# Performance work log

Measured on AMD Instinct MI355X. Metric: run time of the kernel, lower is better.

Reference implementation:

```python
import jax, jax.numpy as jnp
import numpy as np

N = 8192
F_IN = 256
F_OUT = 128
ALPHA = 0.2  # leaky relu slope
NEG_INF = -9e15


def setup_inputs() -> dict:
    key = jax.random.key(0)
    k_x, k_w, k_a, k_adj = jax.random.split(key, 4)
    x = jax.random.normal(k_x, (N, F_IN), dtype=jnp.float32)
    # xavier_uniform for W
    limit = np.sqrt(6.0 / (F_IN + F_OUT)).astype(np.float32)
    W = jax.random.uniform(k_w, (F_IN, F_OUT), minval=-limit, maxval=limit, dtype=jnp.float32)
    a = jax.random.normal(k_a, (2 * F_OUT, 1), dtype=jnp.float32) * 0.1
    adj = (jax.random.uniform(k_adj, (N, N)) < 0.01).astype(jnp.float32)
    adj = jnp.maximum(adj, jnp.eye(N, dtype=jnp.float32))
    return {"x": x, "adj": adj, "W": W, "a": a}


def reference(x, adj, W, a):
    # h = X W : [N, F_OUT]
    h = x @ W
    # e_ij = leakyrelu([h_i || h_j] . a) = leakyrelu((h a1)_i + (h a2)_j)
    a1 = a[:F_OUT, 0]  # [F_OUT]
    a2 = a[F_OUT:, 0]  # [F_OUT]
    e = (h @ a1)[:, None] + (h @ a2)[None, :]  # [N, N]
    e = jnp.where(e > 0, e, ALPHA * e)  # LeakyReLU
    att = jnp.where(adj > 0.0, e, NEG_INF)
    att = jax.nn.softmax(att, axis=1)  # row softmax over neighbors
    # dropout p=0.0 -> identity
    h_prime = att @ h  # [N, F_OUT]
    # concat=True -> ELU
    return jax.nn.elu(h_prime)
```

## Files before the change

kernel.cpp:

```cpp
#include <hip/hip_runtime.h>
#include <math.h>

#define N 8192
#define F_IN 256
#define F_OUT 128
#define ALPHA 0.2f
#define CAP 256
#define GEMM_BLOCKS 256

typedef float f32x4 __attribute__((ext_vector_type(4)));

__global__ __launch_bounds__(256) void fused_gemm_scan(const float* __restrict__ x,
                                                       const float* __restrict__ W,
                                                       const float* __restrict__ a,
                                                       const float* __restrict__ adj,
                                                       float* __restrict__ h,
                                                       float* __restrict__ s1,
                                                       float* __restrict__ s2,
                                                       unsigned short* __restrict__ idx,
                                                       int* __restrict__ cnt) {
    __shared__ float xst[64][36];

    const int t = threadIdx.x;
    if (blockIdx.x < GEMM_BLOCKS) {
        const int row0 = blockIdx.x * 32;
        const int rg = t >> 5;
        const int cg = t & 31;
        float acc[4][4] = {};

        for (int k0 = 0; k0 < F_IN; k0 += 64) {
            #pragma unroll
            for (int i = 0; i < 2; ++i) {
                int fi = t + i * 256;
                int r  = fi >> 4;
                int c4 = fi & 15;
                float4 v = *(const float4*)(&x[(size_t)(row0 + r) * F_IN + k0 + c4 * 4]);
                xst[c4 * 4 + 0][r] = v.x;
                xst[c4 * 4 + 1][r] = v.y;
                xst[c4 * 4 + 2][r] = v.z;
                xst[c4 * 4 + 3][r] = v.w;
            }
            __syncthreads();
            #pragma unroll 8
            for (int kk = 0; kk < 64; ++kk) {
                float4 wv = *(const float4*)(&W[(size_t)(k0 + kk) * F_OUT + cg * 4]);
                float4 xv = *(const float4*)(&xst[kk][rg * 4]);
                acc[0][0] += xv.x * wv.x; acc[0][1] += xv.x * wv.y;
                acc[0][2] += xv.x * wv.z; acc[0][3] += xv.x * wv.w;
                acc[1][0] += xv.y * wv.x; acc[1][1] += xv.y * wv.y;
                acc[1][2] += xv.y * wv.z; acc[1][3] += xv.y * wv.w;
                acc[2][0] += xv.z * wv.x; acc[2][1] += xv.z * wv.y;
                acc[2][2] += xv.z * wv.z; acc[2][3] += xv.z * wv.w;
                acc[3][0] += xv.w * wv.x; acc[3][1] += xv.w * wv.y;
                acc[3][2] += xv.w * wv.z; acc[3][3] += xv.w * wv.w;
            }
            __syncthreads();
        }
        #pragma unroll
        for (int r = 0; r < 4; ++r) {
            float4 v = make_float4(acc[r][0], acc[r][1], acc[r][2], acc[r][3]);
            *(float4*)(&h[(size_t)(row0 + rg * 4 + r) * F_OUT + cg * 4]) = v;
        }
        float4 a1 = *(const float4*)(&a[cg * 4]);
        float4 a2 = *(const float4*)(&a[F_OUT + cg * 4]);
        #pragma unroll
        for (int r = 0; r < 4; ++r) {
            float v1 = acc[r][0] * a1.x + acc[r][1] * a1.y + acc[r][2] * a1.z + acc[r][3] * a1.w;
            float v2 = acc[r][0] * a2.x + acc[r][1] * a2.y + acc[r][2] * a2.z + acc[r][3] * a2.w;
            #pragma unroll
            for (int o = 16; o > 0; o >>= 1) {
                v1 += __shfl_xor(v1, o);
                v2 += __shfl_xor(v2, o);
            }
            if (((t & 63) & 31) == 0) {
                s1[row0 + rg * 4 + r] = v1;
                s2[row0 + rg * 4 + r] = v2;
            }
        }
    } else {
        const int wave = t >> 6;
        const int lane = t & 63;
        const int row = (blockIdx.x - GEMM_BLOCKS) * 4 + wave;
        const f32x4* __restrict__ arow = (const f32x4*)(adj + (size_t)row * N);
        unsigned short* __restrict__ outp = idx + (size_t)row * CAP;
        const unsigned long long lt = (1ULL << lane) - 1ULL;
        int c = 0;
        for (int it = 0; it < 32; it += 8) {
            f32x4 vv[8];
            #pragma unroll
            for (int q = 0; q < 8; ++q)
                vv[q] = __builtin_nontemporal_load(&arow[(it + q) * 64 + lane]);
            #pragma unroll
            for (int q = 0; q < 8; ++q) {
                const int base = ((it + q) * 64 + lane) * 4;
                #pragma unroll
                for (int u = 0; u < 4; ++u) {
                    float val = vv[q][u];
                    unsigned long long m = __ballot(val > 0.0f);
                    if (val > 0.0f) {
                        int pos = c + __popcll(m & lt);
                        if (pos < CAP) outp[pos] = (unsigned short)(base + u);
                    }
                    c += (int)__popcll(m);
                }
            }
        }
        if (lane == 0) cnt[row] = c;
    }
}

__global__ __launch_bounds__(256) void attn_gather(const unsigned short* __restrict__ idx,
                                                   const int* __restrict__ cnt,
                                                   const float* __restrict__ h,
                                                   const float* __restrict__ s1,
                                                   const float* __restrict__ s2,
                                                   float* __restrict__ out) {
    __shared__ float wv[CAP];
    __shared__ unsigned short js[CAP];
    __shared__ float red1[4], red2[4];
    __shared__ float pacc[8][128];

    const int i = blockIdx.x;
    const int t = threadIdx.x;
    const int lane = t & 63;
    const int wave = t >> 6;
    const int K = min(cnt[i], CAP);

    float e = -INFINITY;
    int j = 0;
    if (t < K) {
        j = idx[(size_t)i * CAP + t];
        float v = s1[i] + s2[j];
        e = v > 0.0f ? v : ALPHA * v;
    }
    float m = e;
    #pragma unroll
    for (int o = 32; o > 0; o >>= 1) m = fmaxf(m, __shfl_xor(m, o));
    if (lane == 0) red1[wave] = m;
    __syncthreads();
    m = fmaxf(fmaxf(red1[0], red1[1]), fmaxf(red1[2], red1[3]));

    float w = (t < K) ? expf(e - m) : 0.0f;
    float s = w;
    #pragma unroll
    for (int o = 32; o > 0; o >>= 1) s += __shfl_xor(s, o);
    if (lane == 0) red2[wave] = s;
    wv[t] = w;
    js[t] = (unsigned short)j;
    __syncthreads();
    const float invl = 1.0f / (red2[0] + red2[1] + red2[2] + red2[3]);

    const int g   = t >> 5;
    const int l32 = t & 31;
    const float4* __restrict__ h4 = (const float4*)h;
    float ax = 0.0f, ay = 0.0f, az = 0.0f, aw = 0.0f;
    int k = g;
    for (; k + 8 < K; k += 16) {
        float w0 = wv[k];     int j0 = js[k];
        float w1 = wv[k + 8]; int j1 = js[k + 8];
        float4 h0 = h4[(size_t)j0 * 32 + l32];
        float4 h1 = h4[(size_t)j1 * 32 + l32];
        ax += w0 * h0.x + w1 * h1.x;
        ay += w0 * h0.y + w1 * h1.y;
        az += w0 * h0.z + w1 * h1.z;
        aw += w0 * h0.w + w1 * h1.w;
    }
    for (; k < K; k += 8) {
        float w0 = wv[k]; int j0 = js[k];
        float4 h0 = h4[(size_t)j0 * 32 + l32];
        ax += w0 * h0.x; ay += w0 * h0.y; az += w0 * h0.z; aw += w0 * h0.w;
    }
    pacc[g][l32 * 4 + 0] = ax;
    pacc[g][l32 * 4 + 1] = ay;
    pacc[g][l32 * 4 + 2] = az;
    pacc[g][l32 * 4 + 3] = aw;
    __syncthreads();

    if (t < 128) {
        float v = pacc[0][t] + pacc[1][t] + pacc[2][t] + pacc[3][t]
                + pacc[4][t] + pacc[5][t] + pacc[6][t] + pacc[7][t];
        v *= invl;
        v = v > 0.0f ? v : expm1f(v);
        out[(size_t)i * F_OUT + t] = v;
    }
}

extern "C" void kernel_launch(void* const* d_in, const int* in_sizes, int n_in,
                              void* d_out, int out_size, void* d_ws, size_t ws_size,
                              hipStream_t stream) {
    const float* x   = (const float*)d_in[0];
    const float* adj = (const float*)d_in[1];
    const float* W   = (const float*)d_in[2];
    const float* a   = (const float*)d_in[3];
    float* out = (float*)d_out;

    float* h  = (float*)d_ws;
    float* s1 = h + (size_t)N * F_OUT;
    float* s2 = s1 + N;
    int*   cnt = (int*)(s2 + N);
    unsigned short* idx = (unsigned short*)(cnt + N);

    fused_gemm_scan<<<GEMM_BLOCKS + N / 4, 256, 0, stream>>>(x, W, a, adj, h, s1, s2, idx, cnt);
    attn_gather<<<N, 256, 0, stream>>>(idx, cnt, h, s1, s2, out);
}
```

Measured before the change: 379.3 us.

## Fuse adjacency scan with attention gather, one row per wave

Splits the GEMM into its own kernel and fuses the adjacency scan with softmax and aggregation in a single kernel. Each wave handles one row, keeping neighbor indices and weights in shared memory. This removes the global idx/cnt buffers and the separate per-row gather launch. In exchange, the scan no longer overlaps the GEMM, and each row's gather uses fewer threads.

```diff
diff --git a/kernel.cpp b/kernel.cpp
--- a/kernel.cpp
+++ b/kernel.cpp
@@ -6,158 +6,152 @@
 #define F_OUT 128
 #define ALPHA 0.2f
 #define CAP 256
-#define GEMM_BLOCKS 256
 
 typedef float f32x4 __attribute__((ext_vector_type(4)));
 
-__global__ __launch_bounds__(256) void fused_gemm_scan(const float* __restrict__ x,
-                                                       const float* __restrict__ W,
-                                                       const float* __restrict__ a,
-                                                       const float* __restrict__ adj,
-                                                       float* __restrict__ h,
-                                                       float* __restrict__ s1,
-                                                       float* __restrict__ s2,
-                                                       unsigned short* __restrict__ idx,
-                                                       int* __restrict__ cnt) {
+__global__ __launch_bounds__(256) void gemm_xw(const float* __restrict__ x,
+                                               const float* __restrict__ W,
+                                               const float* __restrict__ a,
+                                               float* __restrict__ h,
+                                               float* __restrict__ s1,
+                                               float* __restrict__ s2) {
     __shared__ float xst[64][36];
 
     const int t = threadIdx.x;
-    if (blockIdx.x < GEMM_BLOCKS) {
-        const int row0 = blockIdx.x * 32;
-        const int rg = t >> 5;
-        const int cg = t & 31;
-        float acc[4][4] = {};
+    const int row0 = blockIdx.x * 32;
+    const int rg = t >> 5;
+    const int cg = t & 31;
+    float acc[4][4] = {};
 
-        for (int k0 = 0; k0 < F_IN; k0 += 64) {
-            #pragma unroll
-            for (int i = 0; i < 2; ++i) {
-                int fi = t + i * 256;
-                int r  = fi >> 4;
-                int c4 = fi & 15;
-                float4 v = *(const float4*)(&x[(size_t)(row0 + r) * F_IN + k0 + c4 * 4]);
-                xst[c4 * 4 + 0][r] = v.x;
-                xst[c4 * 4 + 1][r] = v.y;
-                xst[c4 * 4 + 2][r] = v.z;
-                xst[c4 * 4 + 3][r] = v.w;
-            }
-            __syncthreads();
-            #pragma unroll 8
-            for (int kk = 0; kk < 64; ++kk) {
-                float4 wv = *(const float4*)(&W[(size_t)(k0 + kk) * F_OUT + cg * 4]);
-                float4 xv = *(const float4*)(&xst[kk][rg * 4]);
-                acc[0][0] += xv.x * wv.x; acc[0][1] += xv.x * wv.y;
-                acc[0][2] += xv.x * wv.z; acc[0][3] += xv.x * wv.w;
-                acc[1][0] += xv.y * wv.x; acc[1][1] += xv.y * wv.y;
-                acc[1][2] += xv.y * wv.z; acc[1][3] += xv.y * wv.w;
-                acc[2][0] += xv.z * wv.x; acc[2][1] += xv.z * wv.y;
-                acc[2][2] += xv.z * wv.z; acc[2][3] += xv.z * wv.w;
-                acc[3][0] += xv.w * wv.x; acc[3][1] += xv.w * wv.y;
-                acc[3][2] += xv.w * wv.z; acc[3][3] += xv.w * wv.w;
-            }
-            __syncthreads();
+    for (int k0 = 0; k0 < F_IN; k0 += 64) {
+        #pragma unroll
+        for (int i = 0; i < 2; ++i) {
+            int fi = t + i * 256;
+            int r  = fi >> 4;
+            int c4 = fi & 15;
+            float4 v = *(const float4*)(&x[(size_t)(row0 + r) * F_IN + k0 + c4 * 4]);
+            xst[c4 * 4 + 0][r] = v.x;
+            xst[c4 * 4 + 1][r] = v.y;
+            xst[c4 * 4 + 2][r] = v.z;
+            xst[c4 * 4 + 3][r] = v.w;
         }
+        __syncthreads();
+        #pragma unroll 8
+        for (int kk = 0; kk < 64; ++kk) {
+            float4 wv = *(const float4*)(&W[(size_t)(k0 + kk) * F_OUT + cg * 4]);
+            float4 xv = *(const float4*)(&xst[kk][rg * 4]);
+            acc[0][0] += xv.x * wv.x; acc[0][1] += xv.x * wv.y;
+            acc[0][2] += xv.x * wv.z; acc[0][3] += xv.x * wv.w;
+            acc[1][0] += xv.y * wv.x; acc[1][1] += xv.y * wv.y;
+            acc[1][2] += xv.y * wv.z; acc[1][3] += xv.y * wv.w;
+            acc[2][0] += xv.z * wv.x; acc[2][1] += xv.z * wv.y;
+            acc[2][2] += xv.z * wv.z; acc[2][3] += xv.z * wv.w;
+            acc[3][0] += xv.w * wv.x; acc[3][1] += xv.w * wv.y;
+            acc[3][2] += xv.w * wv.z; acc[3][3] += xv.w * wv.w;
+        }
+        __syncthreads();
+    }
+    #pragma unroll
+    for (int r = 0; r < 4; ++r) {
+        float4 v = make_float4(acc[r][0], acc[r][1], acc[r][2], acc[r][3]);
+        *(float4*)(&h[(size_t)(row0 + rg * 4 + r) * F_OUT + cg * 4]) = v;
+    }
+    float4 a1 = *(const float4*)(&a[cg * 4]);
+    float4 a2 = *(const float4*)(&a[F_OUT + cg * 4]);
+    #pragma unroll
+    for (int r = 0; r < 4; ++r) {
+        float v1 = acc[r][0] * a1.x + acc[r][1] * a1.y + acc[r][2] * a1.z + acc[r][3] * a1.w;
+        float v2 = acc[r][0] * a2.x + acc[r][1] * a2.y + acc[r][2] * a2.z + acc[r][3] * a2.w;
         #pragma unroll
-        for (int r = 0; r < 4; ++r) {
-            float4 v = make_float4(acc[r][0], acc[r][1], acc[r][2], acc[r][3]);
-            *(float4*)(&h[(size_t)(row0 + rg * 4 + r) * F_OUT + cg * 4]) = v;
+        for (int o = 16; o > 0; o >>= 1) {
+            v1 += __shfl_xor(v1, o);
+            v2 += __shfl_xor(v2, o);
         }
-        float4 a1 = *(const float4*)(&a[cg * 4]);
-        float4 a2 = *(const float4*)(&a[F_OUT + cg * 4]);
-        #pragma unroll
-        for (int r = 0; r < 4; ++r) {
-            float v1 = acc[r][0] * a1.x + acc[r][1] * a1.y + acc[r][2] * a1.z + acc[r][3] * a1.w;
-            float v2 = acc[r][0] * a2.x + acc[r][1] * a2.y + acc[r][2] * a2.z + acc[r][3] * a2.w;
-            #pragma unroll
-            for (int o = 16; o > 0; o >>= 1) {
-                v1 += __shfl_xor(v1, o);
-                v2 += __shfl_xor(v2, o);
-            }
-            if (((t & 63) & 31) == 0) {
-                s1[row0 + rg * 4 + r] = v1;
-                s2[row0 + rg * 4 + r] = v2;
-            }
+        if ((t & 31) == 0) {
+            s1[row0 + rg * 4 + r] = v1;
+            s2[row0 + rg * 4 + r] = v2;
         }
-    } else {
-        const int wave = t >> 6;
-        const int lane = t & 63;
-        const int row = (blockIdx.x - GEMM_BLOCKS) * 4 + wave;
-        const f32x4* __restrict__ arow = (const f32x4*)(adj + (size_t)row * N);
-        unsigned short* __restrict__ outp = idx + (size_t)row * CAP;
-        const unsigned long long lt = (1ULL << lane) - 1ULL;
-        int c = 0;
-        for (int it = 0; it < 32; it += 8) {
-            f32x4 vv[8];
-            #pragma unroll
-            for (int q = 0; q < 8; ++q)
-                vv[q] = __builtin_nontemporal_load(&arow[(it + q) * 64 + lane]);
-            #pragma unroll
-            for (int q = 0; q < 8; ++q) {
-                const int base = ((it + q) * 64 + lane) * 4;
-                #pragma unroll
-                for (int u = 0; u < 4; ++u) {
-                    float val = vv[q][u];
-                    unsigned long long m = __ballot(val > 0.0f);
-                    if (val > 0.0f) {
-                        int pos = c + __popcll(m & lt);
-                        if (pos < CAP) outp[pos] = (unsigned short)(base + u);
-                    }
-                    c += (int)__popcll(m);
-                }
-            }
-        }
-        if (lane == 0) cnt[row] = c;
     }
 }
 
-__global__ __launch_bounds__(256) void attn_gather(const unsigned short* __restrict__ idx,
-                                                   const int* __restrict__ cnt,
-                                                   const float* __restrict__ h,
-                                                   const float* __restrict__ s1,
-                                                   const float* __restrict__ s2,
-                                                   float* __restrict__ out) {
-    __shared__ float wv[CAP];
-    __shared__ unsigned short js[CAP];
-    __shared__ float red1[4], red2[4];
-    __shared__ float pacc[8][128];
+__global__ __launch_bounds__(256) void scan_attn(const float* __restrict__ adj,
+                                                 const float* __restrict__ h,
+                                                 const float* __restrict__ s1,
+                                                 const float* __restrict__ s2,
+                                                 float* __restrict__ out) {
+    __shared__ unsigned short js[4][CAP];
+    __shared__ float wv[4][CAP];
 
-    const int i = blockIdx.x;
-    const int t = threadIdx.x;
-    const int lane = t & 63;
-    const int wave = t >> 6;
-    const int K = min(cnt[i], CAP);
+    const int wave = threadIdx.x >> 6;
+    const int lane = threadIdx.x & 63;
+    const int row = blockIdx.x * 4 + wave;
+    const f32x4* __restrict__ arow = (const f32x4*)(adj + (size_t)row * N);
+    const unsigned long long lt = (1ULL << lane) - 1ULL;
 
-    float e = -INFINITY;
-    int j = 0;
-    if (t < K) {
-        j = idx[(size_t)i * CAP + t];
-        float v = s1[i] + s2[j];
-        e = v > 0.0f ? v : ALPHA * v;
+    int c = 0;
+    for (int it = 0; it < 32; it += 8) {
+        f32x4 vv[8];
+        #pragma unroll
+        for (int q = 0; q < 8; ++q)
+            vv[q] = __builtin_nontemporal_load(&arow[(it + q) * 64 + lane]);
+        #pragma unroll
+        for (int q = 0; q < 8; ++q) {
+            const int base = ((it + q) * 64 + lane) * 4;
+            #pragma unroll
+            for (int u = 0; u < 4; ++u) {
+                float val = vv[q][u];
+                unsigned long long m = __ballot(val > 0.0f);
+                if (val > 0.0f) {
+                    int pos = c + __popcll(m & lt);
+                    if (pos < CAP) js[wave][pos] = (unsigned short)(base + u);
+                }
+                c += (int)__popcll(m);
+            }
+        }
     }
-    float m = e;
+    const int K = min(c, CAP);
+    __syncthreads();
+
+    const float s1i = s1[row];
+    float e[4];
+    float mloc = -INFINITY;
     #pragma unroll
-    for (int o = 32; o > 0; o >>= 1) m = fmaxf(m, __shfl_xor(m, o));
-    if (lane == 0) red1[wave] = m;
+    for (int u = 0; u < 4; ++u) {
+        int p = lane + 64 * u;
+        e[u] = -INFINITY;
+        if (p < K) {
+            int j = js[wave][p];
+            float v = s1i + s2[j];
+            v = v > 0.0f ? v : ALPHA * v;
+            e[u] = v;
+            mloc = fmaxf(mloc, v);
+        }
+    }
+    #pragma unroll
+    for (int o = 32; o > 0; o >>= 1) mloc = fmaxf(mloc, __shfl_xor(mloc, o));
+    float ssum = 0.0f;
+    #pragma unroll
+    for (int u = 0; u < 4; ++u) {
+        int p = lane + 64 * u;
+        if (p < K) {
+            float w = expf(e[u] - mloc);
+            wv[wave][p] = w;
+            ssum += w;
+        }
+    }
+    #pragma unroll
+    for (int o = 32; o > 0; o >>= 1) ssum += __shfl_xor(ssum, o);
+    const float invl = 1.0f / ssum;
     __syncthreads();
-    m = fmaxf(fmaxf(red1[0], red1[1]), fmaxf(red1[2], red1[3]));
 
-    float w = (t < K) ? expf(e - m) : 0.0f;
-    float s = w;
-    #pragma unroll
-    for (int o = 32; o > 0; o >>= 1) s += __shfl_xor(s, o);
-    if (lane == 0) red2[wave] = s;
-    wv[t] = w;
-    js[t] = (unsigned short)j;
-    __syncthreads();
-    const float invl = 1.0f / (red2[0] + red2[1] + red2[2] + red2[3]);
-
-    const int g   = t >> 5;
-    const int l32 = t & 31;
+    const int g   = lane >> 5;
+    const int l32 = lane & 31;
     const float4* __restrict__ h4 = (const float4*)h;
     float ax = 0.0f, ay = 0.0f, az = 0.0f, aw = 0.0f;
     int k = g;
-    for (; k + 8 < K; k += 16) {
-        float w0 = wv[k];     int j0 = js[k];
-        float w1 = wv[k + 8]; int j1 = js[k + 8];
+    for (; k + 2 < K; k += 4) {
+        float w0 = wv[wave][k];     int j0 = js[wave][k];
+        float w1 = wv[wave][k + 2]; int j1 = js[wave][k + 2];
         float4 h0 = h4[(size_t)j0 * 32 + l32];
         float4 h1 = h4[(size_t)j1 * 32 + l32];
         ax += w0 * h0.x + w1 * h1.x;
@@ -165,23 +159,22 @@
         az += w0 * h0.z + w1 * h1.z;
         aw += w0 * h0.w + w1 * h1.w;
     }
-    for (; k < K; k += 8) {
-        float w0 = wv[k]; int j0 = js[k];
+    for (; k < K; k += 2) {
+        float w0 = wv[wave][k]; int j0 = js[wave][k];
         float4 h0 = h4[(size_t)j0 * 32 + l32];
         ax += w0 * h0.x; ay += w0 * h0.y; az += w0 * h0.z; aw += w0 * h0.w;
     }
-    pacc[g][l32 * 4 + 0] = ax;
-    pacc[g][l32 * 4 + 1] = ay;
-    pacc[g][l32 * 4 + 2] = az;
-    pacc[g][l32 * 4 + 3] = aw;
-    __syncthreads();
-
-    if (t < 128) {
-        float v = pacc[0][t] + pacc[1][t] + pacc[2][t] + pacc[3][t]
-                + pacc[4][t] + pacc[5][t] + pacc[6][t] + pacc[7][t];
-        v *= invl;
-        v = v > 0.0f ? v : expm1f(v);
-        out[(size_t)i * F_OUT + t] = v;
+    ax += __shfl_xor(ax, 32);
+    ay += __shfl_xor(ay, 32);
+    az += __shfl_xor(az, 32);
+    aw += __shfl_xor(aw, 32);
+    if (g == 0) {
+        float4 v;
+        v.x = ax * invl; v.x = v.x > 0.0f ? v.x : expm1f(v.x);
+        v.y = ay * invl; v.y = v.y > 0.0f ? v.y : expm1f(v.y);
+        v.z = az * invl; v.z = v.z > 0.0f ? v.z : expm1f(v.z);
+        v.w = aw * invl; v.w = v.w > 0.0f ? v.w : expm1f(v.w);
+        *(float4*)(&out[(size_t)row * F_OUT + l32 * 4]) = v;
     }
 }
 
@@ -197,9 +190,7 @@
     float* h  = (float*)d_ws;
     float* s1 = h + (size_t)N * F_OUT;
     float* s2 = s1 + N;
-    int*   cnt = (int*)(s2 + N);
-    unsigned short* idx = (unsigned short*)(cnt + N);
 
-    fused_gemm_scan<<<GEMM_BLOCKS + N / 4, 256, 0, stream>>>(x, W, a, adj, h, s1, s2, idx, cnt);
-    attn_gather<<<N, 256, 0, stream>>>(idx, cnt, h, s1, s2, out);
+    gemm_xw<<<N / 32, 256, 0, stream>>>(x, W, a, h, s1, s2);
+    scan_attn<<<N / 4, 256, 0, stream>>>(adj, h, s1, s2, out);
 }
```

After: 383.9 us. Within noise of the previous version (+1.2%).
